# Kernel optimization log

Hardware: AMD Instinct MI355X
Metric: run time of the kernel (lower is better)

Reference implementation:

```python
import jax, jax.numpy as jnp
import numpy as np

N = 200000   # total nodes across batched graphs
E = 800000   # total edges
B = 4096     # number of graphs
IN = 32      # node feature dim
H1 = 128
D = 64       # set2set / conv3 dim


def setup_inputs():
    key = jax.random.key(0)
    ks = jax.random.split(key, 36)
    def rn(k, shape, s=0.05):
        return jax.random.normal(k, shape, dtype=jnp.float32) * s
    inp = {}
    inp["x"] = jax.random.normal(ks[0], (N, IN), dtype=jnp.float32)
    inp["edge_attr"] = jax.random.uniform(ks[1], (E, 6), dtype=jnp.float32)
    inp["t"] = jax.random.uniform(ks[2], (B, 1), dtype=jnp.float32)
    inp["p"] = jax.random.uniform(ks[3], (B, 1), dtype=jnp.float32)
    inp["e1_w"] = rn(ks[4], (6, IN));    inp["e1_b"] = rn(ks[5], (IN,))
    inp["nn1_w"] = rn(ks[6], (IN, H1));  inp["nn1_b"] = rn(ks[7], (H1,))
    inp["l1_w"] = rn(ks[8], (IN, H1));   inp["l1_b"] = rn(ks[9], (H1,))
    inp["e2_w"] = rn(ks[10], (6, H1));   inp["e2_b"] = rn(ks[11], (H1,))
    inp["nn2_w"] = rn(ks[12], (H1, H1)); inp["nn2_b"] = rn(ks[13], (H1,))
    inp["l2_w"] = rn(ks[14], (H1, H1));  inp["l2_b"] = rn(ks[15], (H1,))
    inp["e3_w"] = rn(ks[16], (6, H1));   inp["e3_b"] = rn(ks[17], (H1,))
    inp["nn3_w"] = rn(ks[18], (H1, D));  inp["nn3_b"] = rn(ks[19], (D,))
    inp["l3_w"] = rn(ks[20], (H1, D));   inp["l3_b"] = rn(ks[21], (D,))
    inp["lstm_wih"] = rn(ks[22], (2 * D, 4 * D))
    inp["lstm_whh"] = rn(ks[23], (D, 4 * D))
    inp["lstm_bih"] = rn(ks[24], (4 * D,))
    inp["lstm_bhh"] = rn(ks[25], (4 * D,))
    inp["l4_w"] = rn(ks[26], (2 * D + 2, H1)); inp["l4_b"] = rn(ks[27], (H1,))
    inp["l5_w"] = rn(ks[28], (H1, 1));         inp["l5_b"] = rn(ks[29], (1,))
    inp["edge_index"] = jax.random.randint(ks[30], (2, E), 0, N)
    inp["batch"] = jnp.sort(jax.random.randint(ks[31], (N,), 0, B))
    inp["num_graphs"] = B
    return inp


def _gine(x, edge_index, edge_attr, ew, eb, nw, nb):
    # PyG GINEConv with eps=0: nn((1+eps)*x_i + sum_j relu(x_j + edge_lin(e_ji)))
    src, dst = edge_index[0], edge_index[1]
    msg = jax.nn.relu(x[src] + edge_attr @ ew + eb)               # [E, d]
    aggr = jax.ops.segment_sum(msg, dst, num_segments=x.shape[0])  # [N, d]
    return (x + aggr) @ nw + nb


def _set2set(x, batch, num_graphs, wih, whh, bih, bhh, steps=3):
    d = x.shape[1]
    h = jnp.zeros((num_graphs, d), x.dtype)
    c = jnp.zeros((num_graphs, d), x.dtype)
    q_star = jnp.zeros((num_graphs, 2 * d), x.dtype)
    for _ in range(steps):
        # single-step LSTM (torch gate order i, f, g, o)
        gates = q_star @ wih + h @ whh + bih + bhh
        i, f, g, o = jnp.split(gates, 4, axis=1)
        c = jax.nn.sigmoid(f) * c + jax.nn.sigmoid(i) * jnp.tanh(g)
        h = jax.nn.sigmoid(o) * jnp.tanh(c)
        q = h
        # segment-wise softmax attention over nodes of each graph
        e = jnp.sum(x * q[batch], axis=1)                           # [N]
        emax = jax.ops.segment_max(e, batch, num_segments=num_graphs)
        a = jnp.exp(e - emax[batch])
        asum = jax.ops.segment_sum(a, batch, num_segments=num_graphs)
        a = a / asum[batch]
        r = jax.ops.segment_sum(a[:, None] * x, batch, num_segments=num_graphs)
        q_star = jnp.concatenate([q, r], axis=1)
    return q_star


def reference(x, edge_attr, t, p, e1_w, e1_b, nn1_w, nn1_b, l1_w, l1_b, e2_w, e2_b, nn2_w, nn2_b, l2_w, l2_b, e3_w, e3_b, nn3_w, nn3_b, l3_w, l3_b, lstm_wih, lstm_whh, lstm_bih, lstm_bhh, l4_w, l4_b, l5_w, l5_b, edge_index, batch, num_graphs):
    h = jax.nn.elu(_gine(x, edge_index, edge_attr, e1_w, e1_b, nn1_w, nn1_b) + x @ l1_w + l1_b)
    h = jax.nn.elu(_gine(h, edge_index, edge_attr, e2_w, e2_b, nn2_w, nn2_b) + h @ l2_w + l2_b)
    h = _gine(h, edge_index, edge_attr, e3_w, e3_b, nn3_w, nn3_b) + h @ l3_w + l3_b
    out = _set2set(h, batch, num_graphs, lstm_wih, lstm_whh, lstm_bih, lstm_bhh)
    out = jnp.concatenate([out, t, p], axis=1)  # [B, 130]
    out = jax.nn.relu(out @ l4_w + l4_b)
    out = out @ l5_w + l5_b
    return out.reshape(-1)
```

## Files before the change

kernel.cpp:

```cpp
#include <hip/hip_runtime.h>
#include <hip/hip_bf16.h>
#include <math.h>

#define DEV __device__ __forceinline__
using u16 = unsigned short;
typedef __attribute__((ext_vector_type(8))) short bf16x8;
typedef __attribute__((ext_vector_type(4))) float f32x4;

DEV float elu1(float x) { return x > 0.f ? x : expm1f(x); }
DEV float sigm(float x) { return 1.f / (1.f + expf(-x)); }
DEV float b2f(u16 v) { return __uint_as_float((unsigned)v << 16); }
DEV u16 f2b(float x) { __hip_bfloat16 b = __float2bfloat16(x); return *reinterpret_cast<u16*>(&b); }

__global__ __launch_bounds__(256) void deg_hist(const int* __restrict__ ei,
                                                int* __restrict__ deg, int E) {
    const int e = blockIdx.x * 256 + threadIdx.x;
    if (e < E) atomicAdd(&deg[ei[E + e]], 1);
}

__global__ __launch_bounds__(256) void scan1(const int* __restrict__ deg,
                                             int* __restrict__ part,
                                             int* __restrict__ bsum, int N) {
    __shared__ int lds[256];
    const int t = threadIdx.x;
    const int base = blockIdx.x * 1024;
    int v[4]; int s = 0;
    #pragma unroll
    for (int k = 0; k < 4; ++k) {
        const int idx = base + t * 4 + k;
        v[k] = (idx < N) ? deg[idx] : 0;
        s += v[k];
    }
    lds[t] = s; __syncthreads();
    int incl = s;
    for (int off = 1; off < 256; off <<= 1) {
        const int add = (t >= off) ? lds[t - off] : 0;
        __syncthreads();
        incl += add; lds[t] = incl;
        __syncthreads();
    }
    if (t == 255) bsum[blockIdx.x] = incl;
    int run = incl - s;
    #pragma unroll
    for (int k = 0; k < 4; ++k) {
        const int idx = base + t * 4 + k;
        if (idx < N) part[idx] = run;
        run += v[k];
    }
}

__global__ __launch_bounds__(256) void scan2(int* __restrict__ bsum, int nb) {
    __shared__ int lds[256];
    __shared__ int carry;
    const int t = threadIdx.x;
    if (t == 0) carry = 0;
    __syncthreads();
    for (int base = 0; base < nb; base += 256) {
        const int idx = base + t;
        const int v = (idx < nb) ? bsum[idx] : 0;
        lds[t] = v; __syncthreads();
        int incl = v;
        for (int off = 1; off < 256; off <<= 1) {
            const int add = (t >= off) ? lds[t - off] : 0;
            __syncthreads();
            incl += add; lds[t] = incl;
            __syncthreads();
        }
        const int c = carry;
        if (idx < nb) bsum[idx] = c + incl - v;
        __syncthreads();
        if (t == 255) carry = c + incl;
        __syncthreads();
    }
}

__global__ __launch_bounds__(256) void scan3(const int* __restrict__ part,
                                             const int* __restrict__ bsum,
                                             int* __restrict__ rowstart,
                                             int* __restrict__ cursor, int N, int E) {
    const int i = blockIdx.x * 256 + threadIdx.x;
    if (i < N) {
        const int v = part[i] + bsum[i >> 10];
        rowstart[i] = v;
        cursor[i] = v;
    }
    if (i == 0) rowstart[N] = E;
}

__global__ __launch_bounds__(256) void edge_scatter(const int* __restrict__ ei,
                                                    const float* __restrict__ eattr,
                                                    int* __restrict__ cursor,
                                                    int* __restrict__ src_s,
                                                    float* __restrict__ eattr_s, int E) {
    const int e = blockIdx.x * 256 + threadIdx.x;
    if (e >= E) return;
    const int src = ei[e], dst = ei[E + e];
    const float2 a0 = *(const float2*)(eattr + (size_t)e * 6);
    const float2 a1 = *(const float2*)(eattr + (size_t)e * 6 + 2);
    const float2 a2 = *(const float2*)(eattr + (size_t)e * 6 + 4);
    const int pos = atomicAdd(&cursor[dst], 1);
    src_s[pos] = src;
    float* ds = eattr_s + (size_t)pos * 6;
    *(float2*)ds = a0; *(float2*)(ds + 2) = a1; *(float2*)(ds + 4) = a2;
}

__global__ __launch_bounds__(256) void build_gstart(const int* __restrict__ batch,
                                                    int* __restrict__ gstart, int N, int B) {
    const int i = blockIdx.x * 256 + threadIdx.x;
    if (i >= N) return;
    const int b = batch[i];
    if (i == 0) for (int g = 0; g <= b; ++g) gstart[g] = 0;
    else {
        const int pb = batch[i - 1];
        for (int g = pb + 1; g <= b; ++g) gstart[g] = i;
    }
    if (i == N - 1) for (int g = b + 1; g <= B; ++g) gstart[g] = N;
}

template<int DIN, int DOUT>
__global__ __launch_bounds__(256) void wcat_prep(
    const float* __restrict__ nnW, const float* __restrict__ lW,
    const float* __restrict__ nnB, const float* __restrict__ lB,
    u16* __restrict__ wswz, float* __restrict__ bcomb)
{
    constexpr int COLT = DOUT / 16;
    const int idx = blockIdx.x * 256 + threadIdx.x;
    if (idx < 2 * DIN * DOUT) {
        const int k = idx / DOUT, n = idx % DOUT;
        const float v = (k < DIN) ? nnW[k * DOUT + n]
                                  : nnW[(k - DIN) * DOUT + n] + lW[(k - DIN) * DOUT + n];
        const int kc = k >> 5, khi = (k >> 3) & 3, j = k & 7;
        const int ct = n >> 4, n16 = n & 15;
        wswz[(size_t)(((kc * COLT + ct) * 4 + khi) * 16 + n16) * 8 + j] = f2b(v);
    }
    if (idx < DOUT) bcomb[idx] = nnB[idx] + lB[idx];
}

__global__ __launch_bounds__(256) void f32_to_bf16v(const float* __restrict__ src,
                                                    u16* __restrict__ dst, int n4) {
    const int i = blockIdx.x * 256 + threadIdx.x;
    if (i >= n4) return;
    const float4 v = *(const float4*)(src + (size_t)i * 4);
    ushort4 u; u.x = f2b(v.x); u.y = f2b(v.y); u.z = f2b(v.z); u.w = f2b(v.w);
    *(ushort4*)(dst + (size_t)i * 4) = u;
}

template<int DIN, int DOUT, bool ELU, typename TOUT>
__global__ __launch_bounds__(256) void fused_layer(
    const float* __restrict__ xf,
    const u16* __restrict__ hb,
    const float* __restrict__ eattr_s, const float* __restrict__ ew, const float* __restrict__ eb,
    const int* __restrict__ rowstart, const int* __restrict__ src_s,
    const u16* __restrict__ wswz, const float* __restrict__ bcomb,
    TOUT* __restrict__ out, int N)
{
    constexpr int KC1  = DIN / 32;
    constexpr int KC_TOT = 2 * KC1;
    constexpr int COLT = DOUT / 16;
    constexpr int CTW  = COLT / 4;
    constexpr int ASTR = (DIN == 32) ? 80 : 272;
    __shared__ char ldsb[64 * 272];
    const int tid = threadIdx.x;
    const int nb  = blockIdx.x * 64;

    if constexpr (DIN == 32) {
        const int j = tid & 31;
        const float w0 = ew[j], w1 = ew[32 + j], w2 = ew[64 + j],
                    w3 = ew[96 + j], w4 = ew[128 + j], w5 = ew[160 + j];
        const float bj = eb[j];
        #pragma unroll 2
        for (int it = 0; it < 8; ++it) {
            const int nl = it * 8 + (tid >> 5);
            const int n = nb + nl;
            if (n < N) {
                const int s0 = rowstart[n], s1 = rowstart[n + 1];
                float accA = 0.f, accB = 0.f;
                int k = s0;
                for (; k + 4 <= s1; k += 4) {
                    int sr[4];
                    #pragma unroll
                    for (int u = 0; u < 4; ++u) sr[u] = src_s[k + u];
                    float xv[4]; float2 ea[4][3];
                    #pragma unroll
                    for (int u = 0; u < 4; ++u) {
                        xv[u] = xf[(size_t)sr[u] * 32 + j];
                        const float* ep = eattr_s + (size_t)(k + u) * 6;
                        ea[u][0] = *(const float2*)ep;
                        ea[u][1] = *(const float2*)(ep + 2);
                        ea[u][2] = *(const float2*)(ep + 4);
                    }
                    #pragma unroll
                    for (int u = 0; u < 4; ++u) {
                        float el = bj;
                        el = fmaf(ea[u][0].x, w0, el); el = fmaf(ea[u][0].y, w1, el);
                        el = fmaf(ea[u][1].x, w2, el); el = fmaf(ea[u][1].y, w3, el);
                        el = fmaf(ea[u][2].x, w4, el); el = fmaf(ea[u][2].y, w5, el);
                        const float m = fmaxf(xv[u] + el, 0.f);
                        if (u & 1) accB += m; else accA += m;
                    }
                }
                for (; k < s1; ++k) {
                    const int sr = src_s[k];
                    const float* ep = eattr_s + (size_t)k * 6;
                    float el = bj;
                    el = fmaf(ep[0], w0, el); el = fmaf(ep[1], w1, el);
                    el = fmaf(ep[2], w2, el); el = fmaf(ep[3], w3, el);
                    el = fmaf(ep[4], w4, el); el = fmaf(ep[5], w5, el);
                    accA += fmaxf(xf[(size_t)sr * 32 + j] + el, 0.f);
                }
                *(u16*)(ldsb + nl * 80 + j * 2) = f2b(accA + accB);
            }
        }
    } else {
        const int lane = tid & 63;
        const int wid  = tid >> 6;
        const int j0 = lane << 1;
        float2 wv[6];
        #pragma unroll
        for (int q = 0; q < 6; ++q) wv[q] = *(const float2*)(ew + q * 128 + j0);
        const float2 bv = *(const float2*)(eb + j0);
        for (int it = 0; it < 16; ++it) {
            const int n = __builtin_amdgcn_readfirstlane(nb + it * 4 + wid);
            const int nl = n - nb;
            if (n < N) {
                const int s0 = rowstart[n], s1 = rowstart[n + 1];
                float a0A = 0.f, a1A = 0.f, a0B = 0.f, a1B = 0.f;
                int k = s0;
                for (; k + 4 <= s1; k += 4) {
                    int sr[4];
                    #pragma unroll
                    for (int u = 0; u < 4; ++u) sr[u] = src_s[k + u];
                    ushort2 xv[4];
                    #pragma unroll
                    for (int u = 0; u < 4; ++u)
                        xv[u] = *(const ushort2*)(hb + (size_t)sr[u] * 128 + j0);
                    #pragma unroll
                    for (int u = 0; u < 4; ++u) {
                        const float* ep = eattr_s + (size_t)(k + u) * 6;
                        const float e0 = ep[0], e1 = ep[1], e2 = ep[2],
                                    e3 = ep[3], e4 = ep[4], e5 = ep[5];
                        float l0 = bv.x, l1 = bv.y;
                        l0 = fmaf(e0, wv[0].x, l0); l1 = fmaf(e0, wv[0].y, l1);
                        l0 = fmaf(e1, wv[1].x, l0); l1 = fmaf(e1, wv[1].y, l1);
                        l0 = fmaf(e2, wv[2].x, l0); l1 = fmaf(e2, wv[2].y, l1);
                        l0 = fmaf(e3, wv[3].x, l0); l1 = fmaf(e3, wv[3].y, l1);
                        l0 = fmaf(e4, wv[4].x, l0); l1 = fmaf(e4, wv[4].y, l1);
                        l0 = fmaf(e5, wv[5].x, l0); l1 = fmaf(e5, wv[5].y, l1);
                        const float m0 = fmaxf(b2f(xv[u].x) + l0, 0.f);
                        const float m1 = fmaxf(b2f(xv[u].y) + l1, 0.f);
                        if (u & 1) { a0B += m0; a1B += m1; } else { a0A += m0; a1A += m1; }
                    }
                }
                for (; k < s1; ++k) {
                    const int sr = src_s[k];
                    const ushort2 xv = *(const ushort2*)(hb + (size_t)sr * 128 + j0);
                    const float* ep = eattr_s + (size_t)k * 6;
                    float l0 = bv.x, l1 = bv.y;
                    l0 = fmaf(ep[0], wv[0].x, l0); l1 = fmaf(ep[0], wv[0].y, l1);
                    l0 = fmaf(ep[1], wv[1].x, l0); l1 = fmaf(ep[1], wv[1].y, l1);
                    l0 = fmaf(ep[2], wv[2].x, l0); l1 = fmaf(ep[2], wv[2].y, l1);
                    l0 = fmaf(ep[3], wv[3].x, l0); l1 = fmaf(ep[3], wv[3].y, l1);
                    l0 = fmaf(ep[4], wv[4].x, l0); l1 = fmaf(ep[4], wv[4].y, l1);
                    l0 = fmaf(ep[5], wv[5].x, l0); l1 = fmaf(ep[5], wv[5].y, l1);
                    a0A += fmaxf(b2f(xv.x) + l0, 0.f);
                    a1A += fmaxf(b2f(xv.y) + l1, 0.f);
                }
                ushort2 o; o.x = f2b(a0A + a0B); o.y = f2b(a1A + a1B);
                *(ushort2*)(ldsb + nl * 272 + j0 * 2) = o;
            }
        }
    }
    __syncthreads();

    const int lane = tid & 63, wid = tid >> 6;
    const int n16 = lane & 15, khi = lane >> 4;
    f32x4 acc[4][CTW];
    #pragma unroll
    for (int g = 0; g < 4; ++g)
        #pragma unroll
        for (int c = 0; c < CTW; ++c) acc[g][c] = (f32x4){0.f, 0.f, 0.f, 0.f};
    #pragma unroll
    for (int kc = 0; kc < KC_TOT; ++kc) {
        bf16x8 bf[CTW];
        #pragma unroll
        for (int c = 0; c < CTW; ++c) {
            const int ct = wid * CTW + c;
            bf[c] = *(const bf16x8*)(wswz + (size_t)(((kc * COLT + ct) * 4 + khi) * 16 + n16) * 8);
        }
        #pragma unroll
        for (int g = 0; g < 4; ++g) {
            bf16x8 af;
            if (kc < KC1) {
                af = *(const bf16x8*)(ldsb + (g * 16 + n16) * ASTR + kc * 64 + khi * 16);
            } else {
                const int row = min(nb + g * 16 + n16, N - 1);
                af = *(const bf16x8*)(hb + (size_t)row * DIN + (kc - KC1) * 32 + khi * 8);
            }
            #pragma unroll
            for (int c = 0; c < CTW; ++c)
                acc[g][c] = __builtin_amdgcn_mfma_f32_16x16x32_bf16(af, bf[c], acc[g][c], 0, 0, 0);
        }
    }
    __syncthreads();

    #pragma unroll
    for (int c = 0; c < CTW; ++c) {
        const int col = (wid * CTW + c) * 16 + n16;
        const float bv = bcomb[col];
        #pragma unroll
        for (int g = 0; g < 4; ++g) {
            #pragma unroll
            for (int r = 0; r < 4; ++r) {
                const int nl = g * 16 + khi * 4 + r;
                float v = acc[g][c][r] + bv;
                if (ELU) v = elu1(v);
                if constexpr (sizeof(TOUT) == 2) *(u16*)(ldsb + nl * 272 + col * 2) = f2b(v);
                else                             *(float*)(ldsb + nl * 272 + col * 4) = v;
            }
        }
    }
    __syncthreads();
    char* outc = (char*)out;
    #pragma unroll
    for (int it = 0; it < 4; ++it) {
        const int task = it * 256 + tid;
        const int row = task >> 4, cch = task & 15;
        if (nb + row < N)
            *(float4*)(outc + (size_t)(nb + row) * (DOUT * sizeof(TOUT)) + cch * 16) =
                *(const float4*)(ldsb + row * 272 + cch * 16);
    }
}

__global__ __launch_bounds__(256) void lstm_gates(
    const float* __restrict__ qstar, const float* __restrict__ hS,
    const float* __restrict__ wih, const float* __restrict__ whh,
    const float* __restrict__ bih, const float* __restrict__ bhh,
    float* __restrict__ gates, int B)
{
    const int idx = blockIdx.x * 256 + threadIdx.x;
    const int g = idx >> 8, jj = idx & 255;
    if (g >= B) return;
    float acc = bih[jj] + bhh[jj];
    const float* q = qstar + g * 128;
    const float* h = hS + g * 64;
    #pragma unroll 4
    for (int k = 0; k < 128; ++k) acc = fmaf(q[k], wih[k * 256 + jj], acc);
    #pragma unroll 4
    for (int k = 0; k < 64;  ++k) acc = fmaf(h[k], whh[k * 256 + jj], acc);
    gates[g * 256 + jj] = acc;
}

__global__ __launch_bounds__(256) void lstm_update(
    const float* __restrict__ gates, float* __restrict__ cS, float* __restrict__ hS, int B)
{
    const int idx = blockIdx.x * 256 + threadIdx.x;
    const int g = idx >> 6, d = idx & 63;
    if (g >= B) return;
    const float i_ = gates[g * 256 + d];
    const float f_ = gates[g * 256 + 64 + d];
    const float g_ = gates[g * 256 + 128 + d];
    const float o_ = gates[g * 256 + 192 + d];
    float c = cS[g * 64 + d];
    c = sigm(f_) * c + sigm(i_) * tanhf(g_);
    cS[g * 64 + d] = c;
    hS[g * 64 + d] = sigm(o_) * tanhf(c);
}

__global__ __launch_bounds__(256) void attn_step(
    const float* __restrict__ h3, const float* __restrict__ hS,
    const int* __restrict__ gstart, float* __restrict__ qstar, int B)
{
    const int g = (blockIdx.x * 256 + threadIdx.x) >> 6;
    const int lane = threadIdx.x & 63;
    if (g >= B) return;
    const float q = hS[g * 64 + lane];
    const int s0 = gstart[g], s1 = gstart[g + 1];
    float m = -INFINITY, ssum = 0.f, racc = 0.f;
    int n = s0;
    for (; n + 2 <= s1; n += 2) {
        const float hv0 = h3[(size_t)n * 64 + lane];
        const float hv1 = h3[(size_t)(n + 1) * 64 + lane];
        float v0 = hv0 * q, v1 = hv1 * q;
        #pragma unroll
        for (int off = 32; off; off >>= 1) {
            v0 += __shfl_xor(v0, off, 64);
            v1 += __shfl_xor(v1, off, 64);
        }
        const float mnew = fmaxf(m, fmaxf(v0, v1));
        const float sc = expf(m - mnew);
        const float a0 = expf(v0 - mnew);
        const float a1 = expf(v1 - mnew);
        ssum = ssum * sc + a0 + a1;
        racc = racc * sc + a0 * hv0 + a1 * hv1;
        m = mnew;
    }
    for (; n < s1; ++n) {
        const float hv = h3[(size_t)n * 64 + lane];
        float v = hv * q;
        #pragma unroll
        for (int off = 32; off; off >>= 1) v += __shfl_xor(v, off, 64);
        const float mnew = fmaxf(m, v);
        const float sc = expf(m - mnew);
        const float a  = expf(v - mnew);
        ssum = ssum * sc + a;
        racc = racc * sc + a * hv;
        m = mnew;
    }
    const float r = (ssum > 0.f) ? racc / ssum : 0.f;
    qstar[g * 128 + lane] = q;
    qstar[g * 128 + 64 + lane] = r;
}

__global__ __launch_bounds__(256) void mlp_hidden(
    const float* __restrict__ qstar, const float* __restrict__ t, const float* __restrict__ p,
    const float* __restrict__ l4w, const float* __restrict__ l4b,
    float* __restrict__ hidden, int B)
{
    const int idx = blockIdx.x * 256 + threadIdx.x;
    const int g = idx >> 7, j = idx & 127;
    if (g >= B) return;
    float acc = l4b[j];
    const float* q = qstar + g * 128;
    #pragma unroll 4
    for (int k = 0; k < 128; ++k) acc = fmaf(q[k], l4w[k * 128 + j], acc);
    acc = fmaf(t[g], l4w[128 * 128 + j], acc);
    acc = fmaf(p[g], l4w[129 * 128 + j], acc);
    hidden[g * 128 + j] = fmaxf(acc, 0.f);
}

__global__ __launch_bounds__(256) void out_proj(
    const float* __restrict__ hidden, const float* __restrict__ l5w,
    const float* __restrict__ l5b, float* __restrict__ dout, int B)
{
    const int wid = (blockIdx.x * 256 + threadIdx.x) >> 6;
    const int lane = threadIdx.x & 63;
    if (wid >= B) return;
    float s = fmaf(hidden[wid * 128 + lane], l5w[lane],
                   hidden[wid * 128 + 64 + lane] * l5w[64 + lane]);
    #pragma unroll
    for (int m = 32; m; m >>= 1) s += __shfl_xor(s, m, 64);
    if (lane == 0) dout[wid] = s + l5b[0];
}

extern "C" void kernel_launch(void* const* d_in, const int* in_sizes, int n_in,
                              void* d_out, int out_size, void* d_ws, size_t ws_size,
                              hipStream_t stream)
{
    const float* x     = (const float*)d_in[0];
    const float* eattr = (const float*)d_in[1];
    const float* t     = (const float*)d_in[2];
    const float* p     = (const float*)d_in[3];
    const float* e1w = (const float*)d_in[4];  const float* e1b = (const float*)d_in[5];
    const float* nn1w= (const float*)d_in[6];  const float* nn1b= (const float*)d_in[7];
    const float* l1w = (const float*)d_in[8];  const float* l1b = (const float*)d_in[9];
    const float* e2w = (const float*)d_in[10]; const float* e2b = (const float*)d_in[11];
    const float* nn2w= (const float*)d_in[12]; const float* nn2b= (const float*)d_in[13];
    const float* l2w = (const float*)d_in[14]; const float* l2b = (const float*)d_in[15];
    const float* e3w = (const float*)d_in[16]; const float* e3b = (const float*)d_in[17];
    const float* nn3w= (const float*)d_in[18]; const float* nn3b= (const float*)d_in[19];
    const float* l3w = (const float*)d_in[20]; const float* l3b = (const float*)d_in[21];
    const float* wih = (const float*)d_in[22]; const float* whh = (const float*)d_in[23];
    const float* bih = (const float*)d_in[24]; const float* bhh = (const float*)d_in[25];
    const float* l4w = (const float*)d_in[26]; const float* l4b = (const float*)d_in[27];
    const float* l5w = (const float*)d_in[28]; const float* l5b = (const float*)d_in[29];
    const int* ei    = (const int*)d_in[30];
    const int* batch = (const int*)d_in[31];
    float* dout = (float*)d_out;

    const int N = in_sizes[0] / 32;
    const int E = in_sizes[30] / 2;
    const int B = in_sizes[2];

    char* basep = (char*)d_ws;
    size_t off = 0;
    auto take = [&](size_t bytes) -> char* {
        char* ptr = basep + off;
        off = (off + bytes + 255) & ~(size_t)255;
        return ptr;
    };
    int* src_s      = (int*)  take((size_t)E * 4);
    float* eattr_s  = (float*)take((size_t)E * 24);
    int* deg      = (int*) take((size_t)N * 4);
    int* part     = (int*) take((size_t)N * 4);
    int* bsum     = (int*) take(4096);
    int* rowstart = (int*) take((size_t)(N + 1) * 4);
    int* cursor   = (int*) take((size_t)N * 4);
    int* gstart   = (int*) take((size_t)(B + 1) * 4);
    u16* h1       = (u16*) take((size_t)N * 128 * 2);
    u16* h2       = (u16*) take((size_t)N * 128 * 2);
    float* h3     = (float*)h1;
    u16* xb       = (u16*) take((size_t)N * 32 * 2);
    u16* w1swz    = (u16*) take((size_t)2 * 32 * 128 * 2);
    u16* w2swz    = (u16*) take((size_t)2 * 128 * 128 * 2);
    u16* w3swz    = (u16*) take((size_t)2 * 128 * 64 * 2);
    float* b1c    = (float*)take(128 * 4);
    float* b2c    = (float*)take(128 * 4);
    float* b3c    = (float*)take(64 * 4);
    float* hS     = (float*)take((size_t)B * 256 * 4);
    float* cS     = hS + (size_t)B * 64;
    float* qstar  = cS + (size_t)B * 64;
    float* gates  = (float*)take((size_t)B * 256 * 4);
    float* hidden = (float*)take((size_t)B * 128 * 4);
    (void)ws_size;

    hipMemsetAsync(deg, 0, (size_t)N * 4, stream);
    deg_hist<<<(E + 255) / 256, 256, 0, stream>>>(ei, deg, E);
    const int NB1 = (N + 1023) / 1024;
    scan1<<<NB1, 256, 0, stream>>>(deg, part, bsum, N);
    scan2<<<1, 256, 0, stream>>>(bsum, NB1);
    scan3<<<(N + 255) / 256, 256, 0, stream>>>(part, bsum, rowstart, cursor, N, E);
    edge_scatter<<<(E + 255) / 256, 256, 0, stream>>>(ei, eattr, cursor, src_s, eattr_s, E);
    build_gstart<<<(N + 255) / 256, 256, 0, stream>>>(batch, gstart, N, B);
    f32_to_bf16v<<<(N * 8 + 255) / 256, 256, 0, stream>>>(x, xb, N * 8);
    wcat_prep<32, 128><<<(2 * 32 * 128 + 255) / 256, 256, 0, stream>>>(nn1w, l1w, nn1b, l1b, w1swz, b1c);
    wcat_prep<128, 128><<<(2 * 128 * 128 + 255) / 256, 256, 0, stream>>>(nn2w, l2w, nn2b, l2b, w2swz, b2c);
    wcat_prep<128, 64><<<(2 * 128 * 64 + 255) / 256, 256, 0, stream>>>(nn3w, l3w, nn3b, l3b, w3swz, b3c);

    const int FB = (N + 63) / 64;
    fused_layer<32, 128, true, u16><<<FB, 256, 0, stream>>>(
        x, xb, eattr_s, e1w, e1b, rowstart, src_s, w1swz, b1c, h1, N);
    fused_layer<128, 128, true, u16><<<FB, 256, 0, stream>>>(
        nullptr, h1, eattr_s, e2w, e2b, rowstart, src_s, w2swz, b2c, h2, N);
    fused_layer<128, 64, false, float><<<FB, 256, 0, stream>>>(
        nullptr, h2, eattr_s, e3w, e3b, rowstart, src_s, w3swz, b3c, h3, N);

    hipMemsetAsync(hS, 0, (size_t)B * 256 * 4, stream);
    for (int step = 0; step < 3; ++step) {
        lstm_gates<<<(B * 256 + 255) / 256, 256, 0, stream>>>(qstar, hS, wih, whh, bih, bhh, gates, B);
        lstm_update<<<(B * 64 + 255) / 256, 256, 0, stream>>>(gates, cS, hS, B);
        attn_step<<<(B * 64 + 255) / 256, 256, 0, stream>>>(h3, hS, gstart, qstar, B);
    }

    mlp_hidden<<<(B * 128 + 255) / 256, 256, 0, stream>>>(qstar, t, p, l4w, l4b, hidden, B);
    out_proj<<<(B * 64 + 255) / 256, 256, 0, stream>>>(hidden, l5w, l5b, dout, B);
}
```

Baseline: 645.6 us.

## Switch 128-wide edge aggregation to edge-parallel LDS atomics per node block

For the 128-dim GINE layers, each wave now takes a strided run of the block's contiguous CSR edge range instead of a node's own edges, and accumulates messages into a 32KB fp32 LDS buffer with atomic adds. A destination-index array is added to the edge scatter for this. The aim is to even out load imbalance from varying node degrees and keep waves busy. In exchange it adds LDS atomics, a zero-fill pass, an fp32-to-bf16 repack pass, extra syncs, and a larger LDS footprint that may reduce occupancy. It also makes a few index computations 64-bit.

After: 1.582 ms. 145% more time.

```diff
diff --git a/kernel.cpp b/kernel.cpp
--- a/kernel.cpp
+++ b/kernel.cpp
@@ -91,6 +91,7 @@
                                                     const float* __restrict__ eattr,
                                                     int* __restrict__ cursor,
                                                     int* __restrict__ src_s,
+                                                    int* __restrict__ dst_s,
                                                     float* __restrict__ eattr_s, int E) {
     const int e = blockIdx.x * 256 + threadIdx.x;
     if (e >= E) return;
@@ -100,6 +101,7 @@
     const float2 a2 = *(const float2*)(eattr + (size_t)e * 6 + 4);
     const int pos = atomicAdd(&cursor[dst], 1);
     src_s[pos] = src;
+    dst_s[pos] = dst;
     float* ds = eattr_s + (size_t)pos * 6;
     *(float2*)ds = a0; *(float2*)(ds + 2) = a1; *(float2*)(ds + 4) = a2;
 }
@@ -147,10 +149,10 @@
 
 template<int DIN, int DOUT, bool ELU, typename TOUT>
 __global__ __launch_bounds__(256) void fused_layer(
-    const float* __restrict__ xf,
-    const u16* __restrict__ hb,
+    const float* __restrict__ xf, const u16* __restrict__ hb,
     const float* __restrict__ eattr_s, const float* __restrict__ ew, const float* __restrict__ eb,
     const int* __restrict__ rowstart, const int* __restrict__ src_s,
+    const int* __restrict__ dst_s,
     const u16* __restrict__ wswz, const float* __restrict__ bcomb,
     TOUT* __restrict__ out, int N)
 {
@@ -159,7 +161,9 @@
     constexpr int COLT = DOUT / 16;
     constexpr int CTW  = COLT / 4;
     constexpr int ASTR = (DIN == 32) ? 80 : 272;
-    __shared__ char ldsb[64 * 272];
+    constexpr int LDSZ = (DIN == 128) ? (64 * 128 * 4) : (64 * 272);
+    __shared__ char ldsraw[LDSZ];
+    char* ldsb = ldsraw;
     const int tid = threadIdx.x;
     const int nb  = blockIdx.x * 64;
 
@@ -211,66 +215,79 @@
                 *(u16*)(ldsb + nl * 80 + j * 2) = f2b(accA + accB);
             }
         }
+        __syncthreads();
     } else {
+        float* aggf = (float*)ldsraw;
         const int lane = tid & 63;
         const int wid  = tid >> 6;
         const int j0 = lane << 1;
+        for (int i = tid; i < 64 * 128; i += 256) aggf[i] = 0.f;
         float2 wv[6];
         #pragma unroll
         for (int q = 0; q < 6; ++q) wv[q] = *(const float2*)(ew + q * 128 + j0);
         const float2 bv = *(const float2*)(eb + j0);
+        __syncthreads();
+        const int e0 = rowstart[nb];
+        const int e1 = rowstart[min(nb + 64, N)];
+        int kb = e0 + wid * 4;
+        for (; kb + 4 <= e1; kb += 16) {
+            int sr[4], dl[4]; ushort2 xv[4];
+            #pragma unroll
+            for (int u = 0; u < 4; ++u) { sr[u] = src_s[kb + u]; dl[u] = dst_s[kb + u] - nb; }
+            #pragma unroll
+            for (int u = 0; u < 4; ++u)
+                xv[u] = *(const ushort2*)(hb + (size_t)sr[u] * 128 + j0);
+            #pragma unroll
+            for (int u = 0; u < 4; ++u) {
+                const float* ep = eattr_s + (size_t)(kb + u) * 6;
+                const float e0f = ep[0], e1f = ep[1], e2f = ep[2],
+                            e3f = ep[3], e4f = ep[4], e5f = ep[5];
+                float l0 = bv.x, l1 = bv.y;
+                l0 = fmaf(e0f, wv[0].x, l0); l1 = fmaf(e0f, wv[0].y, l1);
+                l0 = fmaf(e1f, wv[1].x, l0); l1 = fmaf(e1f, wv[1].y, l1);
+                l0 = fmaf(e2f, wv[2].x, l0); l1 = fmaf(e2f, wv[2].y, l1);
+                l0 = fmaf(e3f, wv[3].x, l0); l1 = fmaf(e3f, wv[3].y, l1);
+                l0 = fmaf(e4f, wv[4].x, l0); l1 = fmaf(e4f, wv[4].y, l1);
+                l0 = fmaf(e5f, wv[5].x, l0); l1 = fmaf(e5f, wv[5].y, l1);
+                const float m0 = fmaxf(b2f(xv[u].x) + l0, 0.f);
+                const float m1 = fmaxf(b2f(xv[u].y) + l1, 0.f);
+                atomicAdd(&aggf[dl[u] * 128 + j0], m0);
+                atomicAdd(&aggf[dl[u] * 128 + j0 + 1], m1);
+            }
+        }
+        for (; kb < e1; ++kb) {
+            const int sr = src_s[kb], dl = dst_s[kb] - nb;
+            const ushort2 xv = *(const ushort2*)(hb + (size_t)sr * 128 + j0);
+            const float* ep = eattr_s + (size_t)kb * 6;
+            float l0 = bv.x, l1 = bv.y;
+            l0 = fmaf(ep[0], wv[0].x, l0); l1 = fmaf(ep[0], wv[0].y, l1);
+            l0 = fmaf(ep[1], wv[1].x, l0); l1 = fmaf(ep[1], wv[1].y, l1);
+            l0 = fmaf(ep[2], wv[2].x, l0); l1 = fmaf(ep[2], wv[2].y, l1);
+            l0 = fmaf(ep[3], wv[3].x, l0); l1 = fmaf(ep[3], wv[3].y, l1);
+            l0 = fmaf(ep[4], wv[4].x, l0); l1 = fmaf(ep[4], wv[4].y, l1);
+            l0 = fmaf(ep[5], wv[5].x, l0); l1 = fmaf(ep[5], wv[5].y, l1);
+            atomicAdd(&aggf[dl * 128 + j0],     fmaxf(b2f(xv.x) + l0, 0.f));
+            atomicAdd(&aggf[dl * 128 + j0 + 1], fmaxf(b2f(xv.y) + l1, 0.f));
+        }
+        __syncthreads();
+        float t0[16], t1[16];
+        #pragma unroll
         for (int it = 0; it < 16; ++it) {
-            const int n = __builtin_amdgcn_readfirstlane(nb + it * 4 + wid);
-            const int nl = n - nb;
-            if (n < N) {
-                const int s0 = rowstart[n], s1 = rowstart[n + 1];
-                float a0A = 0.f, a1A = 0.f, a0B = 0.f, a1B = 0.f;
-                int k = s0;
-                for (; k + 4 <= s1; k += 4) {
-                    int sr[4];
-                    #pragma unroll
-                    for (int u = 0; u < 4; ++u) sr[u] = src_s[k + u];
-                    ushort2 xv[4];
-                    #pragma unroll
-                    for (int u = 0; u < 4; ++u)
-                        xv[u] = *(const ushort2*)(hb + (size_t)sr[u] * 128 + j0);
-                    #pragma unroll
-                    for (int u = 0; u < 4; ++u) {
-                        const float* ep = eattr_s + (size_t)(k + u) * 6;
-                        const float e0 = ep[0], e1 = ep[1], e2 = ep[2],
-                                    e3 = ep[3], e4 = ep[4], e5 = ep[5];
-                        float l0 = bv.x, l1 = bv.y;
-                        l0 = fmaf(e0, wv[0].x, l0); l1 = fmaf(e0, wv[0].y, l1);
-                        l0 = fmaf(e1, wv[1].x, l0); l1 = fmaf(e1, wv[1].y, l1);
-                        l0 = fmaf(e2, wv[2].x, l0); l1 = fmaf(e2, wv[2].y, l1);
-                        l0 = fmaf(e3, wv[3].x, l0); l1 = fmaf(e3, wv[3].y, l1);
-                        l0 = fmaf(e4, wv[4].x, l0); l1 = fmaf(e4, wv[4].y, l1);
-                        l0 = fmaf(e5, wv[5].x, l0); l1 = fmaf(e5, wv[5].y, l1);
-                        const float m0 = fmaxf(b2f(xv[u].x) + l0, 0.f);
-                        const float m1 = fmaxf(b2f(xv[u].y) + l1, 0.f);
-                        if (u & 1) { a0B += m0; a1B += m1; } else { a0A += m0; a1A += m1; }
-                    }
-                }
-                for (; k < s1; ++k) {
-                    const int sr = src_s[k];
-                    const ushort2 xv = *(const ushort2*)(hb + (size_t)sr * 128 + j0);
-                    const float* ep = eattr_s + (size_t)k * 6;
-                    float l0 = bv.x, l1 = bv.y;
-                    l0 = fmaf(ep[0], wv[0].x, l0); l1 = fmaf(ep[0], wv[0].y, l1);
-                    l0 = fmaf(ep[1], wv[1].x, l0); l1 = fmaf(ep[1], wv[1].y, l1);
-                    l0 = fmaf(ep[2], wv[2].x, l0); l1 = fmaf(ep[2], wv[2].y, l1);
-                    l0 = fmaf(ep[3], wv[3].x, l0); l1 = fmaf(ep[3], wv[3].y, l1);
-                    l0 = fmaf(ep[4], wv[4].x, l0); l1 = fmaf(ep[4], wv[4].y, l1);
-                    l0 = fmaf(ep[5], wv[5].x, l0); l1 = fmaf(ep[5], wv[5].y, l1);
-                    a0A += fmaxf(b2f(xv.x) + l0, 0.f);
-                    a1A += fmaxf(b2f(xv.y) + l1, 0.f);
-                }
-                ushort2 o; o.x = f2b(a0A + a0B); o.y = f2b(a1A + a1B);
-                *(ushort2*)(ldsb + nl * 272 + j0 * 2) = o;
-            }
-        }
-    }
-    __syncthreads();
+            const int i = it * 256 + tid;
+            const int row = i >> 6, pr = i & 63;
+            t0[it] = aggf[row * 128 + pr * 2];
+            t1[it] = aggf[row * 128 + pr * 2 + 1];
+        }
+        __syncthreads();
+        #pragma unroll
+        for (int it = 0; it < 16; ++it) {
+            const int i = it * 256 + tid;
+            const int row = i >> 6, pr = i & 63;
+            ushort2 o; o.x = f2b(t0[it]); o.y = f2b(t1[it]);
+            *(ushort2*)(ldsb + row * 272 + pr * 4) = o;
+        }
+        __syncthreads();
+    }
 
     const int lane = tid & 63, wid = tid >> 6;
     const int n16 = lane & 15, khi = lane >> 4;
@@ -420,12 +437,12 @@
     const int g = idx >> 7, j = idx & 127;
     if (g >= B) return;
     float acc = l4b[j];
-    const float* q = qstar + g * 128;
+    const float* q = qstar + (size_t)g * 128;
     #pragma unroll 4
     for (int k = 0; k < 128; ++k) acc = fmaf(q[k], l4w[k * 128 + j], acc);
     acc = fmaf(t[g], l4w[128 * 128 + j], acc);
     acc = fmaf(p[g], l4w[129 * 128 + j], acc);
-    hidden[g * 128 + j] = fmaxf(acc, 0.f);
+    hidden[(size_t)g * 128 + j] = fmaxf(acc, 0.f);
 }
 
 __global__ __launch_bounds__(256) void out_proj(
@@ -435,8 +452,8 @@
     const int wid = (blockIdx.x * 256 + threadIdx.x) >> 6;
     const int lane = threadIdx.x & 63;
     if (wid >= B) return;
-    float s = fmaf(hidden[wid * 128 + lane], l5w[lane],
-                   hidden[wid * 128 + 64 + lane] * l5w[64 + lane]);
+    float s = fmaf(hidden[(size_t)wid * 128 + lane], l5w[lane],
+                   hidden[(size_t)wid * 128 + 64 + lane] * l5w[64 + lane]);
     #pragma unroll
     for (int m = 32; m; m >>= 1) s += __shfl_xor(s, m, 64);
     if (lane == 0) dout[wid] = s + l5b[0];
@@ -479,6 +496,7 @@
         return ptr;
     };
     int* src_s      = (int*)  take((size_t)E * 4);
+    int* dst_s      = (int*)  take((size_t)E * 4);
     float* eattr_s  = (float*)take((size_t)E * 24);
     int* deg      = (int*) take((size_t)N * 4);
     int* part     = (int*) take((size_t)N * 4);
@@ -509,7 +527,7 @@
     scan1<<<NB1, 256, 0, stream>>>(deg, part, bsum, N);
     scan2<<<1, 256, 0, stream>>>(bsum, NB1);
     scan3<<<(N + 255) / 256, 256, 0, stream>>>(part, bsum, rowstart, cursor, N, E);
-    edge_scatter<<<(E + 255) / 256, 256, 0, stream>>>(ei, eattr, cursor, src_s, eattr_s, E);
+    edge_scatter<<<(E + 255) / 256, 256, 0, stream>>>(ei, eattr, cursor, src_s, dst_s, eattr_s, E);
     build_gstart<<<(N + 255) / 256, 256, 0, stream>>>(batch, gstart, N, B);
     f32_to_bf16v<<<(N * 8 + 255) / 256, 256, 0, stream>>>(x, xb, N * 8);
     wcat_prep<32, 128><<<(2 * 32 * 128 + 255) / 256, 256, 0, stream>>>(nn1w, l1w, nn1b, l1b, w1swz, b1c);
@@ -518,11 +536,11 @@
 
     const int FB = (N + 63) / 64;
     fused_layer<32, 128, true, u16><<<FB, 256, 0, stream>>>(
-        x, xb, eattr_s, e1w, e1b, rowstart, src_s, w1swz, b1c, h1, N);
+        x, xb, eattr_s, e1w, e1b, rowstart, src_s, dst_s, w1swz, b1c, h1, N);
     fused_layer<128, 128, true, u16><<<FB, 256, 0, stream>>>(
-        nullptr, h1, eattr_s, e2w, e2b, rowstart, src_s, w2swz, b2c, h2, N);
+        nullptr, h1, eattr_s, e2w, e2b, rowstart, src_s, dst_s, w2swz, b2c, h2, N);
     fused_layer<128, 64, false, float><<<FB, 256, 0, stream>>>(
-        nullptr, h2, eattr_s, e3w, e3b, rowstart, src_s, w3swz, b3c, h3, N);
+        nullptr, h2, eattr_s, e3w, e3b, rowstart, src_s, dst_s, w3swz, b3c, h3, N);
 
     hipMemsetAsync(hS, 0, (size_t)B * 256 * 4, stream);
     for (int step = 0; step < 3; ++step) {
```
